# Optimization experiments

Hardware: AMD Instinct MI355X
Metric: run time of the kernel (lower is better)

The kernel has to match this reference:

```python
import jax, jax.numpy as jnp
import numpy as np

B = 8192
D = 256
TEMP = 0.05
EPS = 1e-5
NORM_EPS = 1e-12  # F.normalize default eps


def _l2norm(x):
    n = jnp.linalg.norm(x, axis=1, keepdims=True)
    return x / jnp.maximum(n, NORM_EPS)


def setup_inputs() -> dict:
    key = jax.random.key(0)
    kq, kk = jax.random.split(key)
    q = jax.random.normal(kq, (B, D), dtype=jnp.float32)
    k = jax.random.normal(kk, (B, D), dtype=jnp.float32)
    return {"q": q, "k": k}


def reference(q, k):
    qn = _l2norm(q)
    kn = _l2norm(k)
    # Only the off-diagonal BxB blocks of the (2B,2B) similarity matrix are
    # used: sim[:B, B:] = qn @ kn.T and sim[B:, :B] = its transpose.
    S = jnp.einsum('id,jd->ij', qn, kn)            # [B, B] cosine sims
    E = jnp.exp(S / TEMP)                          # exp(sim / T)
    d = jnp.diagonal(E)                            # nominator_qk == nominator_kq
    off_sum_rows = E.sum(axis=1) - d               # masked row sums (qk negatives)
    off_sum_cols = E.sum(axis=0) - d               # masked col sums (kq negatives)
    den_qk = d + off_sum_rows
    den_kq = d + off_sum_cols
    loss_qk = jnp.sum(-jnp.log(d / den_qk + EPS)) / B
    loss_kq = jnp.sum(-jnp.log(d / den_kq + EPS)) / B
    return loss_qk + loss_kq
```

## Files before the change

### kernel.cpp

```cpp
#include <hip/hip_runtime.h>
#include <hip/hip_bf16.h>


#define NB 8192
#define ND 256

constexpr float EPS = 1e-5f;
constexpr float EXP2_SCALE = 28.853900817779268f;

typedef float f32x4 __attribute__((ext_vector_type(4)));
typedef int   i32x8 __attribute__((ext_vector_type(8)));


__global__ __launch_bounds__(1024) void norm_pack_kernel(
    const float* __restrict__ q, const float* __restrict__ k,
    uint* __restrict__ qp, uint* __restrict__ kp, float* __restrict__ diag,
    float* __restrict__ out) {
  __shared__ uint lq[16 * 68];
  __shared__ uint lk[16 * 68];
  if (blockIdx.x == 0 && threadIdx.x == 0) out[0] = 0.f;

  const int w    = threadIdx.x >> 6;
  const int lane = threadIdx.x & 63;
  const int row  = blockIdx.x * 16 + w;
  const float4* q4 = reinterpret_cast<const float4*>(q + (size_t)row * ND);
  const float4* k4 = reinterpret_cast<const float4*>(k + (size_t)row * ND);
  float4 qv = q4[lane];
  float4 kv = k4[lane];
  float sq = qv.x * qv.x + qv.y * qv.y + qv.z * qv.z + qv.w * qv.w;
  float sk = kv.x * kv.x + kv.y * kv.y + kv.z * kv.z + kv.w * kv.w;
  float dp = qv.x * kv.x + qv.y * kv.y + qv.z * kv.z + qv.w * kv.w;
#pragma unroll
  for (int m = 1; m < 64; m <<= 1) {
    sq += __shfl_xor(sq, m);
    sk += __shfl_xor(sk, m);
    dp += __shfl_xor(dp, m);
  }
  const float iq = 1.0f / fmaxf(sqrtf(sq), 1e-12f);
  const float ik = 1.0f / fmaxf(sqrtf(sk), 1e-12f);
  int dq = __builtin_amdgcn_cvt_pk_fp8_f32(qv.x * iq, qv.y * iq, 0, false);
  dq = __builtin_amdgcn_cvt_pk_fp8_f32(qv.z * iq, qv.w * iq, dq, true);
  int dk = __builtin_amdgcn_cvt_pk_fp8_f32(kv.x * ik, kv.y * ik, 0, false);
  dk = __builtin_amdgcn_cvt_pk_fp8_f32(kv.z * ik, kv.w * ik, dk, true);
  lq[w * 68 + lane] = (uint)dq;
  lk[w * 68 + lane] = (uint)dk;
  if (lane == 0) diag[row] = __expf(dp * iq * ik * 20.0f);
  __syncthreads();

  const int t = threadIdx.x;
  if (t < 512) {
    const int tt = t & 255;
    const int u  = tt >> 1;
    const int h  = tt & 1;
    const int ul = u & 63;
    const int ks = u >> 6;
    const int src_dw = (ul & 15) * 68 + ks * 32 + (ul >> 4) * 8 + h * 4;
    const uint* Ls = (t < 256) ? lq : lk;
    uint4 v = *reinterpret_cast<const uint4*>(&Ls[src_dw]);
    uint* dst = (t < 256) ? qp : kp;
    reinterpret_cast<uint4*>(dst)[(size_t)blockIdx.x * 256 + tt] = v;
  }
}

#define BT 128

__global__ __launch_bounds__(512, 6) void gemm_exp_reduce_kernel(
    const uint* __restrict__ qp, const uint* __restrict__ kp,
    float* __restrict__ RowP, float* __restrict__ ColP) {
  __shared__ float RS[128 * 5];
  __shared__ float CS[128 * 3];

  const int tid  = threadIdx.x;
  const int lane = tid & 63;
  const int wave = tid >> 6;
  const int wr = wave >> 2;
  const int wc = wave & 3;
  const int l15 = lane & 15;
  const int lhi = lane >> 4;

  const int lid = blockIdx.y * 64 + blockIdx.x;
  const int xcd = lid & 7;
  const int j   = lid >> 3;
  const int rb  = (xcd >> 2) * 32 + (j >> 4);
  const int cb  = (xcd & 3) * 16 + (j & 15);
  const int brow = rb * BT;
  const int bcol = cb * BT;

  const i32x8* qp8 = reinterpret_cast<const i32x8*>(qp);
  const i32x8* kp8 = reinterpret_cast<const i32x8*>(kp);
  const int qg0 = (brow >> 4) + wr * 4;
  const int kg0 = (bcol >> 4) + wc * 2;

  f32x4 acc[2][4];
#pragma unroll
  for (int kg = 0; kg < 2; ++kg)
#pragma unroll
    for (int qg = 0; qg < 4; ++qg)
      acc[kg][qg] = (f32x4){0.f, 0.f, 0.f, 0.f};

#pragma unroll
  for (int ks = 0; ks < 2; ++ks) {
    const i32x8 kf0 = kp8[(size_t)(kg0 + 0) * 128 + ks * 64 + lane];
    const i32x8 kf1 = kp8[(size_t)(kg0 + 1) * 128 + ks * 64 + lane];
#pragma unroll
    for (int qg = 0; qg < 4; ++qg) {
      const i32x8 qf = qp8[(size_t)(qg0 + qg) * 128 + ks * 64 + lane];
      acc[0][qg] = __builtin_amdgcn_mfma_scale_f32_16x16x128_f8f6f4(
          kf0, qf, acc[0][qg], 0, 0, 0, 0x7F7F7F7F, 0, 0x7F7F7F7F);
      acc[1][qg] = __builtin_amdgcn_mfma_scale_f32_16x16x128_f8f6f4(
          kf1, qf, acc[1][qg], 0, 0, 0, 0x7F7F7F7F, 0, 0x7F7F7F7F);
    }
  }

#pragma unroll
  for (int kg = 0; kg < 2; ++kg)
#pragma unroll
    for (int qg = 0; qg < 4; ++qg)
#pragma unroll
      for (int j2 = 0; j2 < 4; ++j2)
        acc[kg][qg][j2] = exp2f(acc[kg][qg][j2] * EXP2_SCALE);

  float rs[4];
#pragma unroll
  for (int qg = 0; qg < 4; ++qg) {
    f32x4 s4 = acc[0][qg] + acc[1][qg];
    float v = (s4[0] + s4[1]) + (s4[2] + s4[3]);
    v += __shfl_xor(v, 16);
    v += __shfl_xor(v, 32);
    rs[qg] = v;
  }
  {
    float val = (lhi == 0) ? rs[0] : (lhi == 1) ? rs[1] : (lhi == 2) ? rs[2] : rs[3];
    RS[(wr * 64 + lhi * 16 + l15) * 5 + wc] = val;
  }

  float c0[4], c1[4];
#pragma unroll
  for (int j2 = 0; j2 < 4; ++j2) {
    c0[j2] = (acc[0][0][j2] + acc[0][1][j2]) + (acc[0][2][j2] + acc[0][3][j2]);
    c1[j2] = (acc[1][0][j2] + acc[1][1][j2]) + (acc[1][2][j2] + acc[1][3][j2]);
  }
  const bool b0 = (l15 & 1), b1 = (l15 & 2), b2 = (l15 & 4);
  float d00, d01, d10, d11;
  {
    float t, u;
    t = b0 ? c0[0] : c0[1]; u = __shfl_xor(t, 1); d00 = (b0 ? c0[1] : c0[0]) + u;
    t = b0 ? c0[2] : c0[3]; u = __shfl_xor(t, 1); d01 = (b0 ? c0[3] : c0[2]) + u;
    t = b0 ? c1[0] : c1[1]; u = __shfl_xor(t, 1); d10 = (b0 ? c1[1] : c1[0]) + u;
    t = b0 ? c1[2] : c1[3]; u = __shfl_xor(t, 1); d11 = (b0 ? c1[3] : c1[2]) + u;
  }
  float e0, e1;
  {
    float t, u;
    t = b1 ? d00 : d01; u = __shfl_xor(t, 2); e0 = (b1 ? d01 : d00) + u;
    t = b1 ? d10 : d11; u = __shfl_xor(t, 2); e1 = (b1 ? d11 : d10) + u;
  }
  float f;
  {
    float t = b2 ? e0 : e1;
    float u = __shfl_xor(t, 4);
    f = (b2 ? e1 : e0) + u;
  }
  f += __shfl_xor(f, 8);
  if (l15 < 8) {
    const int kcol = wc * 32 + (l15 >> 2) * 16 + lhi * 4 + (l15 & 3);
    CS[kcol * 3 + wr] = f;
  }
  __syncthreads();

  if (tid < 128) {
    const float* r = &RS[tid * 5];
    RowP[(size_t)cb * NB + brow + tid] = (r[0] + r[1]) + (r[2] + r[3]);
  } else if (tid < 256) {
    const int t = tid - 128;
    ColP[(size_t)rb * NB + bcol + t] = CS[t * 3 + 0] + CS[t * 3 + 1];
  }
}

__global__ __launch_bounds__(256) void loss_kernel(
    const float* __restrict__ diag, const float* __restrict__ RowP,
    const float* __restrict__ ColP, float* __restrict__ out) {
  const int i = blockIdx.x * 256 + threadIdx.x;
  float rs = 0.f, cs = 0.f;
#pragma unroll 8
  for (int j = 0; j < 64; ++j) {
    rs += RowP[(size_t)j * NB + i];
    cs += ColP[(size_t)j * NB + i];
  }
  const float d = diag[i];
  float acc = -__logf(d / rs + EPS) - __logf(d / cs + EPS);
#pragma unroll
  for (int m = 1; m < 64; m <<= 1) acc += __shfl_xor(acc, m);
  __shared__ float ls[4];
  const int wave = threadIdx.x >> 6;
  if ((threadIdx.x & 63) == 0) ls[wave] = acc;
  __syncthreads();
  if (threadIdx.x == 0)
    atomicAdd(out, (ls[0] + ls[1] + ls[2] + ls[3]) * (1.0f / NB));
}

extern "C" void kernel_launch(void* const* d_in, const int* in_sizes, int n_in,
                              void* d_out, int out_size, void* d_ws, size_t ws_size,
                              hipStream_t stream) {
  const float* q = (const float*)d_in[0];
  const float* k = (const float*)d_in[1];
  char* ws = (char*)d_ws;
  uint*  qp   = (uint*)ws;
  uint*  kp   = (uint*)(ws + (size_t)NB * ND);
  float* diag = (float*)(ws + (size_t)2 * NB * ND);
  float* RowP = diag + NB;
  float* ColP = RowP + 64 * NB;
  float* out  = (float*)d_out;

  norm_pack_kernel<<<NB / 16, 1024, 0, stream>>>(q, k, qp, kp, diag, out);
  gemm_exp_reduce_kernel<<<dim3(64, 64), 512, 0, stream>>>(qp, kp, RowP, ColP);
  loss_kernel<<<32, 256, 0, stream>>>(diag, RowP, ColP, out);
}
```

Measured before the change: 51.94 us.

## Use 4 waves per block with 64x64 per-wave tiles in GEMM-exp kernel

The 128x128 block tile now runs on 4 waves instead of 8, and each wave computes a 64x64 sub-tile (4x4 MFMA groups) instead of 64x32. Each loaded q fragment now feeds four k fragments, which cuts global/L2 fragment loads per MFMA and halves the column-reduction partials across waves. The shuffle reduction tree and the LDS layout are rewritten to match. In exchange each wave holds more accumulator registers and the block has fewer waves, with launch bounds lowered to 256 threads and 4 blocks, which may reduce latency hiding.

New measurement: 48.67 us. 6.3% less time.

```diff
diff --git a/kernel.cpp b/kernel.cpp
--- a/kernel.cpp
+++ b/kernel.cpp
@@ -64,17 +64,17 @@
 
 #define BT 128
 
-__global__ __launch_bounds__(512, 6) void gemm_exp_reduce_kernel(
+__global__ __launch_bounds__(256, 4) void gemm_exp_reduce_kernel(
     const uint* __restrict__ qp, const uint* __restrict__ kp,
     float* __restrict__ RowP, float* __restrict__ ColP) {
-  __shared__ float RS[128 * 5];
+  __shared__ float RS[128 * 3];
   __shared__ float CS[128 * 3];
 
   const int tid  = threadIdx.x;
   const int lane = tid & 63;
   const int wave = tid >> 6;
-  const int wr = wave >> 2;
-  const int wc = wave & 3;
+  const int wr = wave >> 1;
+  const int wc = wave & 1;
   const int l15 = lane & 15;
   const int lhi = lane >> 4;
 
@@ -89,31 +89,33 @@
   const i32x8* qp8 = reinterpret_cast<const i32x8*>(qp);
   const i32x8* kp8 = reinterpret_cast<const i32x8*>(kp);
   const int qg0 = (brow >> 4) + wr * 4;
-  const int kg0 = (bcol >> 4) + wc * 2;
-
-  f32x4 acc[2][4];
-#pragma unroll
-  for (int kg = 0; kg < 2; ++kg)
+  const int kg0 = (bcol >> 4) + wc * 4;
+
+  f32x4 acc[4][4];
+#pragma unroll
+  for (int kg = 0; kg < 4; ++kg)
 #pragma unroll
     for (int qg = 0; qg < 4; ++qg)
       acc[kg][qg] = (f32x4){0.f, 0.f, 0.f, 0.f};
 
 #pragma unroll
   for (int ks = 0; ks < 2; ++ks) {
-    const i32x8 kf0 = kp8[(size_t)(kg0 + 0) * 128 + ks * 64 + lane];
-    const i32x8 kf1 = kp8[(size_t)(kg0 + 1) * 128 + ks * 64 + lane];
+    i32x8 kf[4];
+#pragma unroll
+    for (int kg = 0; kg < 4; ++kg)
+      kf[kg] = kp8[(size_t)(kg0 + kg) * 128 + ks * 64 + lane];
 #pragma unroll
     for (int qg = 0; qg < 4; ++qg) {
       const i32x8 qf = qp8[(size_t)(qg0 + qg) * 128 + ks * 64 + lane];
-      acc[0][qg] = __builtin_amdgcn_mfma_scale_f32_16x16x128_f8f6f4(
-          kf0, qf, acc[0][qg], 0, 0, 0, 0x7F7F7F7F, 0, 0x7F7F7F7F);
-      acc[1][qg] = __builtin_amdgcn_mfma_scale_f32_16x16x128_f8f6f4(
-          kf1, qf, acc[1][qg], 0, 0, 0, 0x7F7F7F7F, 0, 0x7F7F7F7F);
+#pragma unroll
+      for (int kg = 0; kg < 4; ++kg)
+        acc[kg][qg] = __builtin_amdgcn_mfma_scale_f32_16x16x128_f8f6f4(
+            kf[kg], qf, acc[kg][qg], 0, 0, 0, 0x7F7F7F7F, 0, 0x7F7F7F7F);
     }
   }
 
 #pragma unroll
-  for (int kg = 0; kg < 2; ++kg)
+  for (int kg = 0; kg < 4; ++kg)
 #pragma unroll
     for (int qg = 0; qg < 4; ++qg)
 #pragma unroll
@@ -123,7 +125,7 @@
   float rs[4];
 #pragma unroll
   for (int qg = 0; qg < 4; ++qg) {
-    f32x4 s4 = acc[0][qg] + acc[1][qg];
+    f32x4 s4 = (acc[0][qg] + acc[1][qg]) + (acc[2][qg] + acc[3][qg]);
     float v = (s4[0] + s4[1]) + (s4[2] + s4[3]);
     v += __shfl_xor(v, 16);
     v += __shfl_xor(v, 32);
@@ -131,47 +133,52 @@
   }
   {
     float val = (lhi == 0) ? rs[0] : (lhi == 1) ? rs[1] : (lhi == 2) ? rs[2] : rs[3];
-    RS[(wr * 64 + lhi * 16 + l15) * 5 + wc] = val;
-  }
-
-  float c0[4], c1[4];
-#pragma unroll
-  for (int j2 = 0; j2 < 4; ++j2) {
-    c0[j2] = (acc[0][0][j2] + acc[0][1][j2]) + (acc[0][2][j2] + acc[0][3][j2]);
-    c1[j2] = (acc[1][0][j2] + acc[1][1][j2]) + (acc[1][2][j2] + acc[1][3][j2]);
-  }
-  const bool b0 = (l15 & 1), b1 = (l15 & 2), b2 = (l15 & 4);
-  float d00, d01, d10, d11;
+    RS[(wr * 64 + lhi * 16 + l15) * 3 + wc] = val;
+  }
+
+  float c[4][4];
+#pragma unroll
+  for (int kg = 0; kg < 4; ++kg)
+#pragma unroll
+    for (int j2 = 0; j2 < 4; ++j2)
+      c[kg][j2] = (acc[kg][0][j2] + acc[kg][1][j2]) +
+                  (acc[kg][2][j2] + acc[kg][3][j2]);
+  const bool b0 = (l15 & 1), b1 = (l15 & 2), b2 = (l15 & 4), b3 = (l15 & 8);
+  float d[4][2];
+#pragma unroll
+  for (int kg = 0; kg < 4; ++kg) {
+#pragma unroll
+    for (int jh = 0; jh < 2; ++jh) {
+      float t = b0 ? c[kg][jh * 2] : c[kg][jh * 2 + 1];
+      float u = __shfl_xor(t, 1);
+      d[kg][jh] = (b0 ? c[kg][jh * 2 + 1] : c[kg][jh * 2]) + u;
+    }
+  }
+  float e[4];
+#pragma unroll
+  for (int kg = 0; kg < 4; ++kg) {
+    float t = b1 ? d[kg][0] : d[kg][1];
+    float u = __shfl_xor(t, 2);
+    e[kg] = (b1 ? d[kg][1] : d[kg][0]) + u;
+  }
+  float g01, g23;
   {
     float t, u;
-    t = b0 ? c0[0] : c0[1]; u = __shfl_xor(t, 1); d00 = (b0 ? c0[1] : c0[0]) + u;
-    t = b0 ? c0[2] : c0[3]; u = __shfl_xor(t, 1); d01 = (b0 ? c0[3] : c0[2]) + u;
-    t = b0 ? c1[0] : c1[1]; u = __shfl_xor(t, 1); d10 = (b0 ? c1[1] : c1[0]) + u;
-    t = b0 ? c1[2] : c1[3]; u = __shfl_xor(t, 1); d11 = (b0 ? c1[3] : c1[2]) + u;
-  }
-  float e0, e1;
-  {
-    float t, u;
-    t = b1 ? d00 : d01; u = __shfl_xor(t, 2); e0 = (b1 ? d01 : d00) + u;
-    t = b1 ? d10 : d11; u = __shfl_xor(t, 2); e1 = (b1 ? d11 : d10) + u;
+    t = b2 ? e[0] : e[1]; u = __shfl_xor(t, 4); g01 = (b2 ? e[1] : e[0]) + u;
+    t = b2 ? e[2] : e[3]; u = __shfl_xor(t, 4); g23 = (b2 ? e[3] : e[2]) + u;
   }
   float f;
   {
-    float t = b2 ? e0 : e1;
-    float u = __shfl_xor(t, 4);
-    f = (b2 ? e1 : e0) + u;
-  }
-  f += __shfl_xor(f, 8);
-  if (l15 < 8) {
-    const int kcol = wc * 32 + (l15 >> 2) * 16 + lhi * 4 + (l15 & 3);
-    CS[kcol * 3 + wr] = f;
-  }
+    float t = b3 ? g01 : g23;
+    float u = __shfl_xor(t, 8);
+    f = (b3 ? g23 : g01) + u;
+  }
+  CS[(wc * 64 + (l15 >> 2) * 16 + lhi * 4 + (l15 & 3)) * 3 + wr] = f;
   __syncthreads();
 
   if (tid < 128) {
-    const float* r = &RS[tid * 5];
-    RowP[(size_t)cb * NB + brow + tid] = (r[0] + r[1]) + (r[2] + r[3]);
-  } else if (tid < 256) {
+    RowP[(size_t)cb * NB + brow + tid] = RS[tid * 3 + 0] + RS[tid * 3 + 1];
+  } else {
     const int t = tid - 128;
     ColP[(size_t)rb * NB + bcol + t] = CS[t * 3 + 0] + CS[t * 3 + 1];
   }
@@ -213,6 +220,6 @@
   float* out  = (float*)d_out;
 
   norm_pack_kernel<<<NB / 16, 1024, 0, stream>>>(q, k, qp, kp, diag, out);
-  gemm_exp_reduce_kernel<<<dim3(64, 64), 512, 0, stream>>>(qp, kp, RowP, ColP);
+  gemm_exp_reduce_kernel<<<dim3(64, 64), 256, 0, stream>>>(qp, kp, RowP, ColP);
   loss_kernel<<<32, 256, 0, stream>>>(diag, RowP, ColP, out);
 }
```
